# Kernel tuning notes

Measured on AMD Instinct MI355X. Metric: run time of the kernel, lower is better.

Reference implementation:

```python
import jax, jax.numpy as jnp
import numpy as np

HEADS = 16
DIM_HEAD = 64
SCALE = DIM_HEAD ** -0.5


def setup_inputs() -> dict:
    key = jax.random.key(0)
    k1, k2, k3, k4 = jax.random.split(key, 4)
    b, n, dim = 2, 2048, 1024
    inner = HEADS * DIM_HEAD  # 1024
    x = jax.random.normal(k1, (b, n, dim), dtype=jnp.float32)
    # binary keep-mask (multiplicative, as in the original module)
    seq_mask = (jax.random.uniform(k2, (b, n)) < 0.9).astype(jnp.float32)
    # weights stored [in, out] (transpose of torch Linear layout)
    w_qkv = jax.random.normal(k3, (dim, inner * 3), dtype=jnp.float32) * (dim ** -0.5)
    w_out = jax.random.normal(k4, (inner, dim), dtype=jnp.float32) * (inner ** -0.5)
    return {"x": x, "seq_mask": seq_mask, "w_qkv": w_qkv, "w_out": w_out}


def reference(x, seq_mask, w_qkv, w_out):
    b, n, dim = x.shape
    qkv = x @ w_qkv                                   # [b, n, 3*inner]
    q, k, v = jnp.split(qkv, 3, axis=-1)
    split_heads = lambda t: t.reshape(b, n, HEADS, DIM_HEAD).transpose(0, 2, 1, 3)
    q, k, v = split_heads(q), split_heads(k), split_heads(v)  # [b, h, n, d]
    dots = jnp.einsum('bhid,bhjd->bhij', q, k) * SCALE        # [b, h, n, n]
    # multiplicative mask, broadcast over heads and query index i; mask depends on key index j
    dots = dots * seq_mask[:, None, None, :]
    attn = jax.nn.softmax(dots, axis=-1)
    out = jnp.einsum('bhij,bhjd->bhid', attn, v)              # [b, h, n, d]
    out = out.transpose(0, 2, 1, 3).reshape(b, n, HEADS * DIM_HEAD)
    return out @ w_out                                        # dropout p=0 -> identity
```

## Files before the change

kernel.cpp:

```cpp
#include <hip/hip_runtime.h>
#include <hip/hip_bf16.h>

using bf16 = __hip_bfloat16;
typedef __attribute__((ext_vector_type(8))) short short8;
typedef __attribute__((ext_vector_type(4))) float floatx4;
typedef __attribute__((ext_vector_type(16))) float floatx16;

#define MFMA_BF16(a, b, c) __builtin_amdgcn_mfma_f32_16x16x32_bf16((a), (b), (c), 0, 0, 0)
#define MFMA32(a, b, c) __builtin_amdgcn_mfma_f32_32x32x16_bf16((a), (b), (c), 0, 0, 0)

__device__ __forceinline__ void gload_lds16(const bf16* g, bf16* l) {
  __builtin_amdgcn_global_load_lds((__attribute__((address_space(1))) void*)g,
                                   (__attribute__((address_space(3))) void*)l,
                                   16, 0, 0);
}

__device__ __forceinline__ unsigned short bfbits(float f) {
  bf16 b = __float2bfloat16(f);
  return *reinterpret_cast<unsigned short*>(&b);
}

#define KSCALE 0.18033688011112042f

__global__ __launch_bounds__(256)
void probemask_k(const void* __restrict__ msrc, bf16* __restrict__ dst,
                 int* __restrict__ flag) {
  __shared__ int any;
  const int tid = threadIdx.x;
  if (tid == 0) any = 0;
  __syncthreads();
  const unsigned* mw = (const unsigned*)msrc;
  int bad = 0;
#pragma unroll
  for (int i = 0; i < 4; i++) {
    unsigned w = mw[tid * 4 + i];
    if (w != 0u && w != 0x3F800000u) bad = 1;
  }
  if (bad) atomicOr(&any, 1);
  __syncthreads();
  const int isbf = any;
  if (tid == 0) flag[0] = isbf;
  if (isbf) {
#pragma unroll
    for (int i = 0; i < 2; i++)
      ((int4*)dst)[tid * 2 + i] = ((const int4*)msrc)[tid * 2 + i];
  } else {
#pragma unroll
    for (int i = 0; i < 4; i++) {
      float4 v = ((const float4*)msrc)[tid * 4 + i];
      int o = tid * 16 + i * 4;
      dst[o + 0] = __float2bfloat16(v.x);
      dst[o + 1] = __float2bfloat16(v.y);
      dst[o + 2] = __float2bfloat16(v.z);
      dst[o + 3] = __float2bfloat16(v.w);
    }
  }
}

__global__ __launch_bounds__(256)
void prep_k(const void* __restrict__ xsrc, bf16* __restrict__ xb,
            const void* __restrict__ in0, bf16* __restrict__ out0,
            const void* __restrict__ in1, bf16* __restrict__ out1,
            const int* __restrict__ flag) {
  __shared__ bf16 tile[32][33];
  const int isbf = *flag;
  if (blockIdx.x < 4096) {
    if (isbf) return;
    int i = (blockIdx.x * 256 + threadIdx.x) * 4;
    float4 v = ((const float4*)xsrc)[i >> 2];
    xb[i + 0] = __float2bfloat16(v.x);
    xb[i + 1] = __float2bfloat16(v.y);
    xb[i + 2] = __float2bfloat16(v.z);
    xb[i + 3] = __float2bfloat16(v.w);
    return;
  }
  constexpr int R = 1024;
  const int t = blockIdx.x - 4096;
  const int bxi = t & 127;
  const int by = (t >> 7) * 32;
  const void* in;
  bf16* out;
  int C, bx;
  if (bxi < 96) { in = in0; out = out0; C = 3072; bx = bxi * 32; }
  else          { in = in1; out = out1; C = 1024; bx = (bxi - 96) * 32; }
  int tx = threadIdx.x & 31, ty = threadIdx.x >> 5;
#pragma unroll
  for (int i = 0; i < 4; i++) {
    size_t idx = (size_t)(by + ty + i * 8) * C + bx + tx;
    tile[ty + i * 8][tx] =
        isbf ? ((const bf16*)in)[idx] : __float2bfloat16(((const float*)in)[idx]);
  }
  __syncthreads();
#pragma unroll
  for (int i = 0; i < 4; i++)
    out[(size_t)(bx + ty + i * 8) * R + by + tx] = tile[tx][ty + i * 8];
}

template <int MODE>
__global__ __launch_bounds__(256, 2)
void gemm_k(const bf16* __restrict__ A, const bf16* __restrict__ Aalt,
            const bf16* __restrict__ Bt,
            bf16* __restrict__ Qo, bf16* __restrict__ Ko, bf16* __restrict__ Vo,
            void* __restrict__ Co, const bf16* __restrict__ Mk,
            const int* __restrict__ flag) {
  constexpr int K = 1024;
  __shared__ __align__(16) bf16 As[128 * 32];
  __shared__ __align__(16) bf16 Bs[128 * 32];

  const int tid = threadIdx.x;
  const int lane = tid & 63;
  const int wv = tid >> 6;
  const int wm = wv & 1, wn = wv >> 1;
  const int l15 = lane & 15, quad = lane >> 4;

  const int nbx = gridDim.x;
  const int nwg = nbx * gridDim.y;
  int wid = blockIdx.y * nbx + blockIdx.x;
  wid = (wid & 7) * (nwg >> 3) + (wid >> 3);
  const int bm = (wid / nbx) * 128;
  const int bn = (wid % nbx) * 128;

  const int sml = tid >> 2;
  const int sg = (tid & 3) ^ ((sml >> 1) & 3);

  const int isbf = *flag;
  const bf16* Ab = (MODE == 0 && isbf) ? Aalt : A;

  floatx4 acc[4][4] = {};

  for (int k0 = 0; k0 < K; k0 += 32) {
    __syncthreads();
    const bf16* a0 = Ab + (size_t)(bm + sml) * K + k0 + sg * 8;
    gload_lds16(a0, &As[tid * 8]);
    gload_lds16(a0 + (size_t)64 * K, &As[2048 + tid * 8]);
    const bf16* b0 = Bt + (size_t)(bn + sml) * K + k0 + sg * 8;
    gload_lds16(b0, &Bs[tid * 8]);
    gload_lds16(b0 + (size_t)64 * K, &Bs[2048 + tid * 8]);
    __syncthreads();

    short8 af[4], bfr[4];
#pragma unroll
    for (int mi = 0; mi < 4; mi++) {
      int m = wm * 64 + mi * 16 + l15;
      af[mi] = *(const short8*)&As[m * 32 + ((quad ^ ((m >> 1) & 3)) * 8)];
    }
#pragma unroll
    for (int ni = 0; ni < 4; ni++) {
      int n = wn * 64 + ni * 16 + l15;
      bfr[ni] = *(const short8*)&Bs[n * 32 + ((quad ^ ((n >> 1) & 3)) * 8)];
    }
#pragma unroll
    for (int mi = 0; mi < 4; mi++)
#pragma unroll
      for (int ni = 0; ni < 4; ni++)
        acc[mi][ni] = MFMA_BF16(af[mi], bfr[ni], acc[mi][ni]);
  }

#pragma unroll
  for (int mi = 0; mi < 4; mi++) {
    const int row0 = bm + wm * 64 + mi * 16 + quad * 4;
#pragma unroll
    for (int ni = 0; ni < 4; ni++) {
      const int col = bn + wn * 64 + ni * 16 + l15;
      if (MODE == 0) {
        const int sec = col >> 10;
        const int cc = col & 1023;
        const int h = cc >> 6, d = cc & 63;
        const int b_idx = row0 >> 11;
        const int nn0 = row0 & 2047;
        if (sec == 0) {
          bf16* dst = Qo + (size_t)(b_idx * 16 + h) * 131072 + (size_t)nn0 * 64 + d;
#pragma unroll
          for (int r = 0; r < 4; r++) dst[r * 64] = __float2bfloat16(acc[mi][ni][r]);
        } else if (sec == 1) {
          const bf16* mrow = Mk + (size_t)b_idx * 2048 + nn0;
          const int t = nn0 >> 6, kt = (nn0 >> 5) & 1, l31r = nn0 & 31;
          const int g = d >> 3, j = d & 7;
          bf16* dst = Ko + (size_t)(b_idx * 16 + h) * 131072 + t * 4096 + kt * 2048 +
                      (g >> 1) * 512 + (g & 1) * 256 + l31r * 8 + j;
#pragma unroll
          for (int r = 0; r < 4; r++)
            dst[r * 8] = __float2bfloat16(acc[mi][ni][r] * KSCALE *
                                          __bfloat162float(mrow[r]));
        } else {
          const int t = nn0 >> 6;
          const int kl = nn0 & 63;
          const int g = kl >> 3, j0 = kl & 7;
          bf16* dst = Vo + (size_t)(b_idx * 16 + h) * 131072 + t * 4096 +
                      (d >> 5) * 2048 + (g >> 1) * 512 + (g & 1) * 256 + (d & 31) * 8 + j0;
          ushort4 u;
          u.x = bfbits(acc[mi][ni][0]);
          u.y = bfbits(acc[mi][ni][1]);
          u.z = bfbits(acc[mi][ni][2]);
          u.w = bfbits(acc[mi][ni][3]);
          *(ushort4*)dst = u;
        }
      } else {
        if (isbf) {
          bf16* C2 = (bf16*)Co;
#pragma unroll
          for (int r = 0; r < 4; r++)
            C2[(size_t)(row0 + r) * 1024 + col] = __float2bfloat16(acc[mi][ni][r]);
        } else {
          float* C2 = (float*)Co;
#pragma unroll
          for (int r = 0; r < 4; r++)
            C2[(size_t)(row0 + r) * 1024 + col] = acc[mi][ni][r];
        }
      }
    }
  }
}

__global__ __launch_bounds__(512, 4)
void flash_k(const bf16* __restrict__ Q, const bf16* __restrict__ Kp,
             const bf16* __restrict__ Vp, bf16* __restrict__ AO) {
  __shared__ __align__(16) float cb[4 * 64 * 32];
  __shared__ float rbuf[4 * 64];

  const int tid = threadIdx.x;
  const int lane = tid & 63;
  const int l31 = lane & 31;
  const int l5h = lane >> 5;
  const int w = tid >> 6;
  const int rg = w & 3;
  const int half = w >> 2;

  const int bid = blockIdx.x;
  const int wk = (bid & 7) * 64 + (bid >> 3);
  const int qt = wk & 15;
  const int hl = wk >> 4;
  const int b_idx = hl >> 4, h = hl & 15;

  const bf16* Qh = Q + (size_t)hl * 131072;
  const int lo = l5h * 256 + l31 * 8;
  const bf16* kptr = Kp + (size_t)hl * 131072 + (size_t)(half * 16) * 4096 + lo;
  const bf16* vptr = Vp + (size_t)hl * 131072 + (size_t)(half * 16) * 4096 + lo;

  const int qbase = qt * 128 + rg * 32;
  const int qrow = qbase + l31;

  short8 qf[4];
#pragma unroll
  for (int c = 0; c < 4; c++)
    qf[c] = *(const short8*)&Qh[(size_t)qrow * 64 + c * 16 + l5h * 8];

  floatx16 o_acc[2] = {};
  float rsm0 = 0.f, rsm1 = 0.f, rsm2 = 0.f, rsm3 = 0.f;

  short8 kf[4];
#pragma unroll
  for (int c = 0; c < 4; c++) kf[c] = *(const short8*)(kptr + c * 512);

#pragma unroll 1
  for (int it = 0; it < 32; ++it) {
    const int kv = it & 1;

    floatx16 s = {};
    __builtin_amdgcn_s_setprio(1);
#pragma unroll
    for (int c = 0; c < 4; c++) s = MFMA32(kf[c], qf[c], s);
    __builtin_amdgcn_s_setprio(0);

    short8 vf[4];
#pragma unroll
    for (int dt = 0; dt < 2; dt++)
#pragma unroll
      for (int ch = 0; ch < 2; ch++)
        vf[dt * 2 + ch] = *(const short8*)(vptr + dt * 2048 + (kv * 2 + ch) * 512);

    kptr += (it < 31) ? 2048 : 0;
#pragma unroll
    for (int c = 0; c < 4; c++) kf[c] = *(const short8*)(kptr + c * 512);

    float e[16];
#pragma unroll
    for (int r = 0; r < 16; r += 4) {
      e[r + 0] = __builtin_amdgcn_exp2f(s[r + 0]);
      e[r + 1] = __builtin_amdgcn_exp2f(s[r + 1]);
      e[r + 2] = __builtin_amdgcn_exp2f(s[r + 2]);
      e[r + 3] = __builtin_amdgcn_exp2f(s[r + 3]);
      rsm0 += e[r + 0];
      rsm1 += e[r + 1];
      rsm2 += e[r + 2];
      rsm3 += e[r + 3];
    }

    short8 pf[2];
#pragma unroll
    for (int ch = 0; ch < 2; ch++) {
      const int rb = ch * 8;
      unsigned x0, x1, y0, y1;
      asm("v_cvt_pk_bf16_f32 %0, %1, %2" : "=v"(x0) : "v"(e[rb + 0]), "v"(e[rb + 1]));
      asm("v_cvt_pk_bf16_f32 %0, %1, %2" : "=v"(x1) : "v"(e[rb + 2]), "v"(e[rb + 3]));
      asm("v_cvt_pk_bf16_f32 %0, %1, %2" : "=v"(y0) : "v"(e[rb + 4]), "v"(e[rb + 5]));
      asm("v_cvt_pk_bf16_f32 %0, %1, %2" : "=v"(y1) : "v"(e[rb + 6]), "v"(e[rb + 7]));
      asm("v_permlane32_swap_b32 %0, %1" : "+v"(x0), "+v"(y0));
      asm("v_permlane32_swap_b32 %0, %1" : "+v"(x1), "+v"(y1));
      union { unsigned u[4]; short8 v; } cv;
      cv.u[0] = x0; cv.u[1] = x1; cv.u[2] = y0; cv.u[3] = y1;
      pf[ch] = cv.v;
    }

    __builtin_amdgcn_s_setprio(1);
#pragma unroll
    for (int dt = 0; dt < 2; dt++)
#pragma unroll
      for (int ch = 0; ch < 2; ch++)
        o_acc[dt] = MFMA32(vf[dt * 2 + ch], pf[ch], o_acc[dt]);
    __builtin_amdgcn_s_setprio(0);

    vptr += kv ? 4096 : 0;
  }

  float rsum = (rsm0 + rsm1) + (rsm2 + rsm3);
  rsum += __shfl_xor(rsum, 32, 64);

  if (w >= 4) {
    const int slot = (w - 4) * 64 + lane;
    float4* dst = (float4*)(cb + (size_t)slot * 32);
#pragma unroll
    for (int dt = 0; dt < 2; dt++)
#pragma unroll
      for (int q = 0; q < 4; q++) {
        float4 v = make_float4(o_acc[dt][q * 4 + 0], o_acc[dt][q * 4 + 1],
                               o_acc[dt][q * 4 + 2], o_acc[dt][q * 4 + 3]);
        dst[(dt * 4 + q) ^ (lane & 7)] = v;
      }
    rbuf[slot] = rsum;
  }
  __syncthreads();
  if (w < 4) {
    const int slot = w * 64 + lane;
    const float4* src = (const float4*)(cb + (size_t)slot * 32);
#pragma unroll
    for (int dt = 0; dt < 2; dt++)
#pragma unroll
      for (int q = 0; q < 4; q++) {
        float4 v = src[(dt * 4 + q) ^ (lane & 7)];
        o_acc[dt][q * 4 + 0] += v.x;
        o_acc[dt][q * 4 + 1] += v.y;
        o_acc[dt][q * 4 + 2] += v.z;
        o_acc[dt][q * 4 + 3] += v.w;
      }
    rsum += rbuf[slot];

    const float rinv = 1.f / rsum;
    bf16* orow = AO + (size_t)(b_idx * 2048 + qbase + l31) * 1024 + h * 64;
#pragma unroll
    for (int dt = 0; dt < 2; dt++)
#pragma unroll
      for (int rg2 = 0; rg2 < 4; rg2++) {
        ushort4 u;
        u.x = bfbits(o_acc[dt][rg2 * 4 + 0] * rinv);
        u.y = bfbits(o_acc[dt][rg2 * 4 + 1] * rinv);
        u.z = bfbits(o_acc[dt][rg2 * 4 + 2] * rinv);
        u.w = bfbits(o_acc[dt][rg2 * 4 + 3] * rinv);
        *(ushort4*)&orow[dt * 32 + rg2 * 8 + l5h * 4] = u;
      }
  }
}

extern "C" void kernel_launch(void* const* d_in, const int* in_sizes, int n_in,
                              void* d_out, int out_size, void* d_ws, size_t ws_size,
                              hipStream_t stream) {
  const void* x     = d_in[0];
  const void* mask  = d_in[1];
  const void* w_qkv = d_in[2];
  const void* w_out = d_in[3];

  bf16* ws    = (bf16*)d_ws;
  bf16* xb    = ws;
  bf16* AO    = ws;
  bf16* wqkvT = ws + 4194304;
  bf16* woutT = wqkvT + 3145728;
  bf16* Qb    = woutT + 1048576;
  bf16* Kp    = Qb + 4194304;
  bf16* maskb = Kp + 4194304;
  int*  flag  = (int*)(maskb + 4096);
  bf16* Vp    = (bf16*)d_out;

  probemask_k<<<1, 256, 0, stream>>>(mask, maskb, flag);
  prep_k<<<8192, 256, 0, stream>>>(x, xb, w_qkv, wqkvT, w_out, woutT, flag);
  gemm_k<0><<<dim3(24, 32), 256, 0, stream>>>(xb, (const bf16*)x, wqkvT, Qb, Kp, Vp,
                                              nullptr, maskb, flag);
  flash_k<<<512, 512, 0, stream>>>(Qb, Kp, Vp, AO);
  gemm_k<1><<<dim3(8, 32), 256, 0, stream>>>(AO, nullptr, woutT, nullptr, nullptr,
                                             nullptr, d_out, nullptr, flag);
}
```

Baseline: 188.6 us.

## Fuse mask probe into prep kernel and double GEMM K-step to 64

Merges the single-block mask probe/convert kernel into the prep kernel: every block recomputes the dtype probe locally and one extra block writes the converted mask and flag, removing one launch and the dependency on the flag. The GEMM now loads two 32-wide K slices per iteration into doubled LDS tiles, halving the number of barrier pairs per K loop. Each prep block now re-reads 4KB of mask, and the larger LDS footprint may affect occupancy.

```diff
diff --git a/kernel.cpp b/kernel.cpp
--- a/kernel.cpp
+++ b/kernel.cpp
@@ -23,9 +23,13 @@
 #define KSCALE 0.18033688011112042f
 
 __global__ __launch_bounds__(256)
-void probemask_k(const void* __restrict__ msrc, bf16* __restrict__ dst,
-                 int* __restrict__ flag) {
+void prep_k(const void* __restrict__ msrc, bf16* __restrict__ maskb,
+            int* __restrict__ flag,
+            const void* __restrict__ xsrc, bf16* __restrict__ xb,
+            const void* __restrict__ in0, bf16* __restrict__ out0,
+            const void* __restrict__ in1, bf16* __restrict__ out1) {
   __shared__ int any;
+  __shared__ bf16 tile[32][33];
   const int tid = threadIdx.x;
   if (tid == 0) any = 0;
   __syncthreads();
@@ -33,40 +37,36 @@
   int bad = 0;
 #pragma unroll
   for (int i = 0; i < 4; i++) {
-    unsigned w = mw[tid * 4 + i];
-    if (w != 0u && w != 0x3F800000u) bad = 1;
+    unsigned w_ = mw[tid * 4 + i];
+    if (w_ != 0u && w_ != 0x3F800000u) bad = 1;
   }
   if (bad) atomicOr(&any, 1);
   __syncthreads();
   const int isbf = any;
-  if (tid == 0) flag[0] = isbf;
-  if (isbf) {
-#pragma unroll
-    for (int i = 0; i < 2; i++)
-      ((int4*)dst)[tid * 2 + i] = ((const int4*)msrc)[tid * 2 + i];
-  } else {
-#pragma unroll
-    for (int i = 0; i < 4; i++) {
-      float4 v = ((const float4*)msrc)[tid * 4 + i];
-      int o = tid * 16 + i * 4;
-      dst[o + 0] = __float2bfloat16(v.x);
-      dst[o + 1] = __float2bfloat16(v.y);
-      dst[o + 2] = __float2bfloat16(v.z);
-      dst[o + 3] = __float2bfloat16(v.w);
-    }
-  }
-}
-
-__global__ __launch_bounds__(256)
-void prep_k(const void* __restrict__ xsrc, bf16* __restrict__ xb,
-            const void* __restrict__ in0, bf16* __restrict__ out0,
-            const void* __restrict__ in1, bf16* __restrict__ out1,
-            const int* __restrict__ flag) {
-  __shared__ bf16 tile[32][33];
-  const int isbf = *flag;
+
+  if (blockIdx.x == 8192) {
+    if (tid == 0) flag[0] = isbf;
+    if (isbf) {
+#pragma unroll
+      for (int i = 0; i < 2; i++)
+        ((int4*)maskb)[tid * 2 + i] = ((const int4*)msrc)[tid * 2 + i];
+    } else {
+#pragma unroll
+      for (int i = 0; i < 4; i++) {
+        float4 v = ((const float4*)msrc)[tid * 4 + i];
+        int o = tid * 16 + i * 4;
+        maskb[o + 0] = __float2bfloat16(v.x);
+        maskb[o + 1] = __float2bfloat16(v.y);
+        maskb[o + 2] = __float2bfloat16(v.z);
+        maskb[o + 3] = __float2bfloat16(v.w);
+      }
+    }
+    return;
+  }
+
   if (blockIdx.x < 4096) {
     if (isbf) return;
-    int i = (blockIdx.x * 256 + threadIdx.x) * 4;
+    int i = (blockIdx.x * 256 + tid) * 4;
     float4 v = ((const float4*)xsrc)[i >> 2];
     xb[i + 0] = __float2bfloat16(v.x);
     xb[i + 1] = __float2bfloat16(v.y);
@@ -74,6 +74,7 @@
     xb[i + 3] = __float2bfloat16(v.w);
     return;
   }
+
   constexpr int R = 1024;
   const int t = blockIdx.x - 4096;
   const int bxi = t & 127;
@@ -83,7 +84,7 @@
   int C, bx;
   if (bxi < 96) { in = in0; out = out0; C = 3072; bx = bxi * 32; }
   else          { in = in1; out = out1; C = 1024; bx = (bxi - 96) * 32; }
-  int tx = threadIdx.x & 31, ty = threadIdx.x >> 5;
+  int tx = tid & 31, ty = tid >> 5;
 #pragma unroll
   for (int i = 0; i < 4; i++) {
     size_t idx = (size_t)(by + ty + i * 8) * C + bx + tx;
@@ -104,8 +105,8 @@
             void* __restrict__ Co, const bf16* __restrict__ Mk,
             const int* __restrict__ flag) {
   constexpr int K = 1024;
-  __shared__ __align__(16) bf16 As[128 * 32];
-  __shared__ __align__(16) bf16 Bs[128 * 32];
+  __shared__ __align__(16) bf16 As[128 * 64];
+  __shared__ __align__(16) bf16 Bs[128 * 64];
 
   const int tid = threadIdx.x;
   const int lane = tid & 63;
@@ -128,32 +129,40 @@
 
   floatx4 acc[4][4] = {};
 
-  for (int k0 = 0; k0 < K; k0 += 32) {
+  for (int k0 = 0; k0 < K; k0 += 64) {
     __syncthreads();
-    const bf16* a0 = Ab + (size_t)(bm + sml) * K + k0 + sg * 8;
-    gload_lds16(a0, &As[tid * 8]);
-    gload_lds16(a0 + (size_t)64 * K, &As[2048 + tid * 8]);
-    const bf16* b0 = Bt + (size_t)(bn + sml) * K + k0 + sg * 8;
-    gload_lds16(b0, &Bs[tid * 8]);
-    gload_lds16(b0 + (size_t)64 * K, &Bs[2048 + tid * 8]);
+#pragma unroll
+    for (int hf = 0; hf < 2; hf++) {
+      const bf16* a0 = Ab + (size_t)(bm + sml) * K + k0 + hf * 32 + sg * 8;
+      gload_lds16(a0, &As[hf * 4096 + tid * 8]);
+      gload_lds16(a0 + (size_t)64 * K, &As[hf * 4096 + 2048 + tid * 8]);
+      const bf16* b0 = Bt + (size_t)(bn + sml) * K + k0 + hf * 32 + sg * 8;
+      gload_lds16(b0, &Bs[hf * 4096 + tid * 8]);
+      gload_lds16(b0 + (size_t)64 * K, &Bs[hf * 4096 + 2048 + tid * 8]);
+    }
     __syncthreads();
 
-    short8 af[4], bfr[4];
-#pragma unroll
-    for (int mi = 0; mi < 4; mi++) {
-      int m = wm * 64 + mi * 16 + l15;
-      af[mi] = *(const short8*)&As[m * 32 + ((quad ^ ((m >> 1) & 3)) * 8)];
-    }
-#pragma unroll
-    for (int ni = 0; ni < 4; ni++) {
-      int n = wn * 64 + ni * 16 + l15;
-      bfr[ni] = *(const short8*)&Bs[n * 32 + ((quad ^ ((n >> 1) & 3)) * 8)];
-    }
-#pragma unroll
-    for (int mi = 0; mi < 4; mi++)
-#pragma unroll
-      for (int ni = 0; ni < 4; ni++)
-        acc[mi][ni] = MFMA_BF16(af[mi], bfr[ni], acc[mi][ni]);
+#pragma unroll
+    for (int hf = 0; hf < 2; hf++) {
+      const bf16* Ah = &As[hf * 4096];
+      const bf16* Bh = &Bs[hf * 4096];
+      short8 af[4], bfr[4];
+#pragma unroll
+      for (int mi = 0; mi < 4; mi++) {
+        int m = wm * 64 + mi * 16 + l15;
+        af[mi] = *(const short8*)&Ah[m * 32 + ((quad ^ ((m >> 1) & 3)) * 8)];
+      }
+#pragma unroll
+      for (int ni = 0; ni < 4; ni++) {
+        int n = wn * 64 + ni * 16 + l15;
+        bfr[ni] = *(const short8*)&Bh[n * 32 + ((quad ^ ((n >> 1) & 3)) * 8)];
+      }
+#pragma unroll
+      for (int mi = 0; mi < 4; mi++)
+#pragma unroll
+        for (int ni = 0; ni < 4; ni++)
+          acc[mi][ni] = MFMA_BF16(af[mi], bfr[ni], acc[mi][ni]);
+    }
   }
 
 #pragma unroll
@@ -380,8 +389,8 @@
   int*  flag  = (int*)(maskb + 4096);
   bf16* Vp    = (bf16*)d_out;
 
-  probemask_k<<<1, 256, 0, stream>>>(mask, maskb, flag);
-  prep_k<<<8192, 256, 0, stream>>>(x, xb, w_qkv, wqkvT, w_out, woutT, flag);
+  prep_k<<<8193, 256, 0, stream>>>(mask, maskb, flag, x, xb, w_qkv, wqkvT,
+                                   w_out, woutT);
   gemm_k<0><<<dim3(24, 32), 256, 0, stream>>>(xb, (const bf16*)x, wqkvT, Qb, Kp, Vp,
                                               nullptr, maskb, flag);
   flash_k<<<512, 512, 0, stream>>>(Qb, Kp, Vp, AO);
```

Result: faster. 183.5 us, median of 3 (-2.7%).
